# Kernel tuning notes

Measured on AMD Instinct MI355X. Metric: run time of the kernel, lower is better.

The kernel has to match this reference:

```python
import jax, jax.numpy as jnp
import numpy as np

EPS = 1e-12

def _l1_normalize(x, axis=1):
    # torch.nn.functional.normalize(p=1): x / max(||x||_1, eps)
    n = jnp.sum(jnp.abs(x), axis=axis, keepdims=True)
    return x / jnp.maximum(n, EPS)

def setup_inputs() -> dict:
    key = jax.random.key(0)
    k1, k2 = jax.random.split(key)
    B, M, C = 8192, 16, 345
    y_pred = jax.random.normal(k1, (B, 1, M * C), dtype=jnp.float32)
    labels = jax.random.randint(k2, (B,), 0, C, dtype=jnp.int64)
    return {"y_pred": y_pred, "labels": labels, "class_type": C, "model_num": M, "num_local": 4}

def reference(y_pred, labels, class_type, model_num, num_local):
    B = y_pred.shape[0]
    M, C = model_num, class_type
    logits = y_pred.reshape(B, M, C)  # y_pred.squeeze(1), split into per-model blocks
    rows = jnp.arange(B)

    # per-model softmax over classes (softmax_multi_child_pred)
    probs = jax.nn.softmax(logits, axis=-1)  # [B, M, C]
    # gather per-sample true-class prob for each model: probs[i, :, labels[i]] -> [B, M]
    true_p = probs[rows, :, labels]
    true_confs = jax.lax.stop_gradient(jax.nn.softmax(true_p, axis=1))  # detached

    # use_true_conf=True -> weights = true_confs
    weights = true_confs

    # num_local < model_num: topk select + scatter + L1 normalize (post_weights)
    vals, idx = jax.lax.top_k(weights, num_local)  # [B, k]
    post = jnp.zeros_like(weights).at[rows[:, None], idx].set(vals)
    post_weights = _l1_normalize(post, axis=1)

    weighted_mat = _l1_normalize(weights, axis=1)

    # strided weighted ensemble sum: sum_m y_pred[:, i::C] * w  ==  einsum over models
    ems_out = jnp.einsum('bmc,bm->bc', logits, weighted_mat)
    ems_out_post = jnp.einsum('bmc,bm->bc', logits, post_weights)

    # per-model, per-sample cross entropy (reduction='none')
    logp = jax.nn.log_softmax(logits, axis=-1)
    each_point_loss = -logp[rows, :, labels]  # [B, M]

    # BCEWithLogitsLoss(softmax(weighted_mat), softmax(true_confs))
    x = jax.nn.softmax(weighted_mat, axis=-1)
    t = jax.nn.softmax(true_confs, axis=-1)
    confidence_loss = jnp.mean(jnp.maximum(x, 0.0) - x * t + jnp.log1p(jnp.exp(-jnp.abs(x))))

    wm_soft = jax.nn.softmax(weighted_mat, axis=-1)
    child_loss = jnp.mean(each_point_loss * wm_soft)

    ensemble_loss = jnp.mean(-jax.nn.log_softmax(ems_out, axis=-1)[rows, labels])

    return (ems_out_post, child_loss, confidence_loss, ensemble_loss, wm_soft, true_confs)
```

## Files before the change

kernel.cpp:

```cpp
#include <hip/hip_runtime.h>
#include <math.h>

#define MM 16
#define CC 345
#define MC (MM*CC)
#define KTOP 4
#define GAP_THR 3e-7f
#define NT 512

__device__ __forceinline__ float fexp(float x) { return __expf(x); }
__device__ __forceinline__ float flog(float x) { return __logf(x); }

__device__ __forceinline__ float rmax16(float v) {
    #pragma unroll
    for (int off = 8; off; off >>= 1) v = fmaxf(v, __shfl_xor(v, off, 16));
    return v;
}
__device__ __forceinline__ float rmin16(float v) {
    #pragma unroll
    for (int off = 8; off; off >>= 1) v = fminf(v, __shfl_xor(v, off, 16));
    return v;
}
__device__ __forceinline__ float rsum16(float v) {
    #pragma unroll
    for (int off = 8; off; off >>= 1) v += __shfl_xor(v, off, 16);
    return v;
}
__device__ __forceinline__ float rmax32(float v) {
    #pragma unroll
    for (int off = 16; off; off >>= 1) v = fmaxf(v, __shfl_xor(v, off, 32));
    return v;
}
__device__ __forceinline__ float rsum32(float v) {
    #pragma unroll
    for (int off = 16; off; off >>= 1) v += __shfl_xor(v, off, 32);
    return v;
}

__global__ __launch_bounds__(NT)
void ens_main(const float* __restrict__ y, const int* __restrict__ labels,
              float* __restrict__ out, float* __restrict__ partial, int B)
{
    const int b   = blockIdx.x;
    const int tid = threadIdx.x;

    __shared__ float sl[MC + 64];
    __shared__ float sems[CC];
    __shared__ float s_truep[MM], s_epl[MM], s_mx[MM], s_tpp[MM];
    __shared__ float s_w[MM], s_pw[MM];
    __shared__ float s_red[NT/64];
    __shared__ int   s_need;
    __shared__ unsigned s_selmask;

    {
        const float4* src = reinterpret_cast<const float4*>(y + (size_t)b * MC);
        float4* dst = reinterpret_cast<float4*>(sl);
        for (int i = tid; i < MC/4; i += NT) dst[i] = src[i];
    }
    __syncthreads();

    const int label = labels[b];

    {
        const int m = tid >> 5;
        const int l = tid & 31;
        const float* row = sl + m * CC;
        float v[11];
        float mx = -INFINITY;
        #pragma unroll
        for (int k = 0; k < 11; ++k) {
            const int c = l + (k << 5);
            if (c < CC) { v[k] = row[c]; mx = fmaxf(mx, v[k]); }
            else          v[k] = 0.f;
        }
        mx = rmax32(mx);
        float se = 0.f;
        #pragma unroll
        for (int k = 0; k < 11; ++k) {
            const int c = l + (k << 5);
            if (c < CC) se += fexp(v[k] - mx);
        }
        se = rsum32(se);
        if (l == 0) {
            const float lt = row[label];
            s_mx[m]    = mx;
            s_truep[m] = fexp(lt - mx) / se;
            s_epl[m]   = -(lt - mx - flog(se));
        }
    }
    __syncthreads();

    float tc = 0.f, wm = 0.f;
    bool  sel = false;
    if (tid < MM) {
        const int l = tid;
        const float tp = s_truep[l];
        const float mx = rmax16(tp);
        const float e  = fexp(tp - mx);
        tc = e / rsum16(e);
        const float s1 = fmaxf(rsum16(fabsf(tc)), 1e-12f);
        wm = tc / s1;
        int rank = 0;
        #pragma unroll
        for (int j = 0; j < MM; ++j) {
            const float vj = __shfl(tc, j, 16);
            rank += (vj > tc) || (vj == tc && j < l);
        }
        sel = (rank < KTOP);
        const float val4 = rmin16(sel ? tc : INFINITY);
        const float val5 = rmax16(sel ? -INFINITY : tc);
        if (l == 0) s_need = (val4 - val5 < GAP_THR) ? 1 : 0;
    }
    __syncthreads();

    if (s_need) {
        if (tid < 256) {
            const int m = tid >> 4;
            const int l = tid & 15;
            const float* row = sl + m * CC;
            const float mx = s_mx[m];
            float se = 0.f;
            for (int c = l; c < CC; c += 16) se += expf(row[c] - mx);
            se = rsum16(se);
            if (l == 0) s_tpp[m] = expf(row[label] - mx) / se;
        }
        __syncthreads();
        if (tid == 0) {
            float tcp[MM];
            float mxx = -INFINITY;
            for (int m = 0; m < MM; ++m) mxx = fmaxf(mxx, s_tpp[m]);
            float ses = 0.f;
            for (int m = 0; m < MM; ++m) { tcp[m] = expf(s_tpp[m] - mxx); ses += tcp[m]; }
            for (int m = 0; m < MM; ++m) tcp[m] /= ses;
            bool used[MM];
            for (int m = 0; m < MM; ++m) used[m] = false;
            unsigned msk = 0;
            for (int k = 0; k < KTOP; ++k) {
                int bi = -1; float bv = -INFINITY;
                for (int m = 0; m < MM; ++m)
                    if (!used[m] && tcp[m] > bv) { bv = tcp[m]; bi = m; }
                used[bi] = true; msk |= (1u << bi);
            }
            s_selmask = msk;
        }
        __syncthreads();
    }

    if (tid < MM) {
        const int l = tid;
        const size_t off_wm = (size_t)B * CC + 3;
        const size_t off_tc = off_wm + (size_t)B * MM;

        if (s_need) sel = ((s_selmask >> l) & 1u) != 0;

        const float post = sel ? tc : 0.f;
        const float psum = fmaxf(rsum16(fabsf(post)), 1e-12f);
        const float pw   = post / psum;
        const float mw = rmax16(wm);
        const float ex = fexp(wm - mw);
        const float xv = ex / rsum16(ex);
        const float mt = rmax16(tc);
        const float et = fexp(tc - mt);
        const float tv = et / rsum16(et);
        const float childp = s_epl[l] * xv;
        const float confp  = fmaxf(xv, 0.f) - xv * tv + flog(1.f + fexp(-fabsf(xv)));
        const float childs = rsum16(childp);
        const float confs  = rsum16(confp);
        if (l == 0) {
            partial[(size_t)b * 3 + 0] = childs;
            partial[(size_t)b * 3 + 1] = confs;
        }
        s_w[l]  = wm;
        s_pw[l] = pw;
        out[off_wm + (size_t)b * MM + l] = xv;
        out[off_tc + (size_t)b * MM + l] = tc;
    }
    __syncthreads();

    {
        const int c = tid;
        const bool act = (c < CC);
        float a = 0.f;
        if (act) {
            float aa = 0.f, ap = 0.f;
            #pragma unroll
            for (int m = 0; m < MM; ++m) {
                const float vv = sl[m * CC + c];
                aa = fmaf(vv, s_w[m],  aa);
                ap = fmaf(vv, s_pw[m], ap);
            }
            sems[c] = aa;
            out[(size_t)b * CC + c] = ap;
            a = aa;
        }
        float e = act ? fexp(a) : 0.f;
        #pragma unroll
        for (int off = 32; off; off >>= 1) e += __shfl_xor(e, off);
        if ((tid & 63) == 0) s_red[tid >> 6] = e;
        __syncthreads();
        if (tid == 0) {
            float s = 0.f;
            #pragma unroll
            for (int w = 0; w < NT/64; ++w) s += s_red[w];
            partial[(size_t)b * 3 + 2] = -(sems[label] - flog(s));
        }
    }
}

__global__ __launch_bounds__(64)
void ens_reduce1(const float* __restrict__ partial, double* __restrict__ ws2, int B)
{
    const int t  = threadIdx.x;
    const int i  = blockIdx.x;
    const int r0 = i * 128 + t * 2;
    double c = 0.0, f = 0.0, e = 0.0;
    #pragma unroll
    for (int k = 0; k < 2; ++k) {
        const int r = r0 + k;
        c += (double)partial[(size_t)r * 3 + 0];
        f += (double)partial[(size_t)r * 3 + 1];
        e += (double)partial[(size_t)r * 3 + 2];
    }
    #pragma unroll
    for (int off = 32; off; off >>= 1) {
        c += __shfl_xor(c, off);
        f += __shfl_xor(f, off);
        e += __shfl_xor(e, off);
    }
    if (t == 0) {
        ws2[(size_t)i * 3 + 0] = c;
        ws2[(size_t)i * 3 + 1] = f;
        ws2[(size_t)i * 3 + 2] = e;
    }
}

__global__ __launch_bounds__(64)
void ens_reduce2(const double* __restrict__ ws2, float* __restrict__ out, int B)
{
    const int t = threadIdx.x;
    double c = ws2[(size_t)t * 3 + 0];
    double f = ws2[(size_t)t * 3 + 1];
    double e = ws2[(size_t)t * 3 + 2];
    #pragma unroll
    for (int off = 32; off; off >>= 1) {
        c += __shfl_xor(c, off);
        f += __shfl_xor(f, off);
        e += __shfl_xor(e, off);
    }
    if (t == 0) {
        const size_t base = (size_t)B * CC;
        out[base + 0] = (float)(c / (double)((size_t)B * MM));
        out[base + 1] = (float)(f / (double)((size_t)B * MM));
        out[base + 2] = (float)(e / (double)B);
    }
}

extern "C" void kernel_launch(void* const* d_in, const int* in_sizes, int n_in,
                              void* d_out, int out_size, void* d_ws, size_t ws_size,
                              hipStream_t stream)
{
    const float* y      = (const float*)d_in[0];
    const int*   labels = (const int*)d_in[1];
    const int    B      = in_sizes[1];
    float* out     = (float*)d_out;
    float* partial = (float*)d_ws;
    double* ws2    = (double*)((char*)d_ws + (((size_t)B * 3 * sizeof(float) + 255) & ~(size_t)255));

    ens_main<<<dim3(B), dim3(NT), 0, stream>>>(y, labels, out, partial, B);
    ens_reduce1<<<dim3(64), dim3(64), 0, stream>>>(partial, ws2, B);
    ens_reduce2<<<dim3(1), dim3(64), 0, stream>>>(ws2, out, B);
}
```

Measured before the change: 62.56 us.

## Load rows directly from global and run tie-break top-k inside one wavefront

Drops the separate float4 global-to-LDS staging pass and its barrier, so each thread loads its softmax row elements straight from global memory and writes them into shared memory as it goes. The near-tie fallback (precise expf recomputation and top-k re-selection) now runs inside a single 64-lane wave using shuffles instead of extra block-wide barriers and a serial single-thread loop. This cuts the number of __syncthreads and serial work per block. The cost is scalar uncoalesced-ish global loads in place of vectorized float4 copies, and the rare tie path now reads global memory again.

```diff
diff --git a/kernel.cpp b/kernel.cpp
--- a/kernel.cpp
+++ b/kernel.cpp
@@ -46,31 +46,24 @@
 
     __shared__ float sl[MC + 64];
     __shared__ float sems[CC];
-    __shared__ float s_truep[MM], s_epl[MM], s_mx[MM], s_tpp[MM];
+    __shared__ float s_truep[MM], s_epl[MM], s_mx[MM];
     __shared__ float s_w[MM], s_pw[MM];
     __shared__ float s_red[NT/64];
-    __shared__ int   s_need;
-    __shared__ unsigned s_selmask;
-
-    {
-        const float4* src = reinterpret_cast<const float4*>(y + (size_t)b * MC);
-        float4* dst = reinterpret_cast<float4*>(sl);
-        for (int i = tid; i < MC/4; i += NT) dst[i] = src[i];
-    }
-    __syncthreads();
 
     const int label = labels[b];
+    const float* yb = y + (size_t)b * MC;
 
     {
         const int m = tid >> 5;
         const int l = tid & 31;
-        const float* row = sl + m * CC;
+        const float* row = yb + m * CC;
+        float* srow = sl + m * CC;
         float v[11];
         float mx = -INFINITY;
         #pragma unroll
         for (int k = 0; k < 11; ++k) {
             const int c = l + (k << 5);
-            if (c < CC) { v[k] = row[c]; mx = fmaxf(mx, v[k]); }
+            if (c < CC) { v[k] = row[c]; srow[c] = v[k]; mx = fmaxf(mx, v[k]); }
             else          v[k] = 0.f;
         }
         mx = rmax32(mx);
@@ -90,68 +83,66 @@
     }
     __syncthreads();
 
-    float tc = 0.f, wm = 0.f;
-    bool  sel = false;
-    if (tid < MM) {
-        const int l = tid;
-        const float tp = s_truep[l];
-        const float mx = rmax16(tp);
-        const float e  = fexp(tp - mx);
-        tc = e / rsum16(e);
-        const float s1 = fmaxf(rsum16(fabsf(tc)), 1e-12f);
-        wm = tc / s1;
+    if (tid < 64) {
+        const int l  = tid;
+        const int lm = l & 15;
+        const int mq = l >> 4;
+        const int g  = l & 15;
+
+        const float tpv  = s_truep[lm];
+        const float eplv = s_epl[lm];
+
+        const float mxs = rmax16(tpv);
+        const float e0  = fexp(tpv - mxs);
+        const float tc  = e0 / rsum16(e0);
+        const float s1  = fmaxf(rsum16(fabsf(tc)), 1e-12f);
+        const float wm  = tc / s1;
         int rank = 0;
         #pragma unroll
         for (int j = 0; j < MM; ++j) {
             const float vj = __shfl(tc, j, 16);
-            rank += (vj > tc) || (vj == tc && j < l);
-        }
-        sel = (rank < KTOP);
+            rank += (vj > tc) || (vj == tc && j < lm);
+        }
+        bool sel = (rank < KTOP);
         const float val4 = rmin16(sel ? tc : INFINITY);
         const float val5 = rmax16(sel ? -INFINITY : tc);
-        if (l == 0) s_need = (val4 - val5 < GAP_THR) ? 1 : 0;
-    }
-    __syncthreads();
-
-    if (s_need) {
-        if (tid < 256) {
-            const int m = tid >> 4;
-            const int l = tid & 15;
-            const float* row = sl + m * CC;
-            const float mx = s_mx[m];
-            float se = 0.f;
-            for (int c = l; c < CC; c += 16) se += expf(row[c] - mx);
-            se = rsum16(se);
-            if (l == 0) s_tpp[m] = expf(row[label] - mx) / se;
-        }
-        __syncthreads();
-        if (tid == 0) {
-            float tcp[MM];
-            float mxx = -INFINITY;
-            for (int m = 0; m < MM; ++m) mxx = fmaxf(mxx, s_tpp[m]);
+        const bool need = (val4 - val5 < GAP_THR);
+
+        if (need) {
+            float tpp4[4];
+            #pragma unroll
+            for (int i = 0; i < 4; ++i) {
+                const int m = i * 4 + mq;
+                const float* row = yb + m * CC;
+                const float mx = s_mx[m];
+                float se = 0.f;
+                for (int c = g; c < CC; c += 16) se += expf(row[c] - mx);
+                se = rsum16(se);
+                tpp4[i] = expf(row[label] - mx) / se;
+            }
+            float tppv = 0.f;
+            {
+                const int src = (lm & 3) << 4;
+                #pragma unroll
+                for (int i = 0; i < 4; ++i) {
+                    const float a_ = __shfl(tpp4[i], src, 64);
+                    if ((lm >> 2) == i) tppv = a_;
+                }
+            }
+            const float mxx = rmax16(tppv);
+            const float ev  = expf(tppv - mxx);
             float ses = 0.f;
-            for (int m = 0; m < MM; ++m) { tcp[m] = expf(s_tpp[m] - mxx); ses += tcp[m]; }
-            for (int m = 0; m < MM; ++m) tcp[m] /= ses;
-            bool used[MM];
-            for (int m = 0; m < MM; ++m) used[m] = false;
-            unsigned msk = 0;
-            for (int k = 0; k < KTOP; ++k) {
-                int bi = -1; float bv = -INFINITY;
-                for (int m = 0; m < MM; ++m)
-                    if (!used[m] && tcp[m] > bv) { bv = tcp[m]; bi = m; }
-                used[bi] = true; msk |= (1u << bi);
-            }
-            s_selmask = msk;
-        }
-        __syncthreads();
-    }
-
-    if (tid < MM) {
-        const int l = tid;
-        const size_t off_wm = (size_t)B * CC + 3;
-        const size_t off_tc = off_wm + (size_t)B * MM;
-
-        if (s_need) sel = ((s_selmask >> l) & 1u) != 0;
+            #pragma unroll
+            for (int m = 0; m < MM; ++m) ses += __shfl(ev, m, 16);
+            const float tcpv = ev / ses;
+            int rk = 0;
+            #pragma unroll
+            for (int j = 0; j < MM; ++j) {
+                const float vj = __shfl(tcpv, j, 16);
+                rk += (vj > tcpv) || (vj == tcpv && j < lm);
+            }
+            sel = (rk < KTOP);
+        }
 
         const float post = sel ? tc : 0.f;
         const float psum = fmaxf(rsum16(fabsf(post)), 1e-12f);
@@ -162,7 +153,7 @@
         const float mt = rmax16(tc);
         const float et = fexp(tc - mt);
         const float tv = et / rsum16(et);
-        const float childp = s_epl[l] * xv;
+        const float childp = eplv * xv;
         const float confp  = fmaxf(xv, 0.f) - xv * tv + flog(1.f + fexp(-fabsf(xv)));
         const float childs = rsum16(childp);
         const float confs  = rsum16(confp);
@@ -170,10 +161,14 @@
             partial[(size_t)b * 3 + 0] = childs;
             partial[(size_t)b * 3 + 1] = confs;
         }
-        s_w[l]  = wm;
-        s_pw[l] = pw;
-        out[off_wm + (size_t)b * MM + l] = xv;
-        out[off_tc + (size_t)b * MM + l] = tc;
+        if (l < MM) {
+            const size_t off_wm = (size_t)B * CC + 3;
+            const size_t off_tc = off_wm + (size_t)B * MM;
+            out[off_wm + (size_t)b * MM + l] = xv;
+            out[off_tc + (size_t)b * MM + l] = tc;
+            s_w[l]  = wm;
+            s_pw[l] = pw;
+        }
     }
     __syncthreads();
 
```

Measured after the change: 73.44 us. 1.17x slower.
